# Kernel optimization log

Measured on AMD Instinct MI355X. Metric: run time of the kernel, lower is better.

Reference implementation:

```python
import jax, jax.numpy as jnp
import numpy as np

N = 100_000   # nodes
E = 1_250_000 # edges
D = 64        # feature dim


def setup_inputs() -> dict:
    key = jax.random.key(0)
    k1, k2, k3, k4 = jax.random.split(key, 4)
    x = jax.random.normal(k1, (N, D), dtype=jnp.float32)
    edge_index = jax.random.randint(k2, (2, E), 0, N, dtype=jnp.int32)
    s = 1.0 / np.sqrt(D)  # glorot-ish scale
    W1 = jax.random.uniform(k3, (D, D), minval=-s, maxval=s, dtype=jnp.float32)
    W2 = jax.random.uniform(k4, (D, D), minval=-s, maxval=s, dtype=jnp.float32)
    b1 = jnp.zeros((D,), jnp.float32)
    b2 = jnp.zeros((D,), jnp.float32)
    return {"x": x, "edge_index": edge_index, "W1": W1, "b1": b1, "W2": W2, "b2": b2}


def gcn_conv(x, edge_index, W, b):
    # PyG GCNConv: add self-loops, symmetric normalization D^-1/2 A D^-1/2,
    # linear transform, scatter-add aggregation over destination nodes.
    n = x.shape[0]
    src, dst = edge_index[0], edge_index[1]
    xw = x @ W  # [N, D]
    deg = jax.ops.segment_sum(jnp.ones((edge_index.shape[1],), x.dtype), dst,
                              num_segments=n) + 1.0  # +1 for self-loop
    inv_sqrt = jax.lax.rsqrt(deg)  # [N]
    coef = inv_sqrt[src] * inv_sqrt[dst]  # [E]
    agg = jax.ops.segment_sum(xw[src] * coef[:, None], dst, num_segments=n)
    # self-loop contribution: coef_ii = deg_i^-1
    agg = agg + xw * (inv_sqrt * inv_sqrt)[:, None]
    return agg + b


def reference(x, edge_index, W1, b1, W2, b2):
    h = jax.nn.relu(gcn_conv(x, edge_index, W1, b1))
    # dropout p=0.6 is identity in eval mode (training=False)
    out = gcn_conv(h, edge_index, W2, b2)
    return jax.nn.log_softmax(out, axis=1)
```

## Files before the change

kernel.cpp:

```cpp
#include <hip/hip_runtime.h>

#define DD 64
#define BSH 8
#define NB_MAX 512
#define SCAP 4096
#define BIN_CH 4096

typedef __attribute__((ext_vector_type(8))) short bf16x8;
typedef __attribute__((ext_vector_type(4))) float f32x4;
union Frag { bf16x8 v; uint32_t d[4]; };

__device__ __forceinline__ float bf_lo(uint32_t d) { return __uint_as_float(d << 16); }
__device__ __forceinline__ float bf_hi(uint32_t d) { return __uint_as_float(d & 0xffff0000u); }
__device__ __forceinline__ float bf2f(uint32_t h) { return __uint_as_float(h << 16); }
__device__ __forceinline__ uint32_t f2bf(float f) {
    uint32_t u = __float_as_uint(f);
    u += 0x7fffu + ((u >> 16) & 1u);
    return u >> 16;
}

__global__ __launch_bounds__(256) void bin_kernel(const int* __restrict__ src,
                                                  const int* __restrict__ dst,
                                                  int* __restrict__ bcnt,
                                                  uint32_t* __restrict__ staging,
                                                  int E, int NB) {
    __shared__ uint32_t sorted[BIN_CH];
    __shared__ int cnt[NB_MAX];
    __shared__ int loc[NB_MAX];
    __shared__ int resv[NB_MAX];
    __shared__ int wsum[4][2];
    int tid = threadIdx.x;
    int lane = tid & 63, wv = tid >> 6;
    int base = blockIdx.x * BIN_CH;
    int cE = min(BIN_CH, E - base);

    cnt[tid] = 0; cnt[tid + 256] = 0;
    __syncthreads();
    for (int k = tid; k < cE; k += 256)
        atomicAdd(&cnt[dst[base + k] >> BSH], 1);
    __syncthreads();
    int v0 = cnt[tid], v1 = cnt[tid + 256];
    int s0 = v0, s1 = v1;
#pragma unroll
    for (int o = 1; o < 64; o <<= 1) {
        int t0 = __shfl_up(s0, o, 64);
        int t1 = __shfl_up(s1, o, 64);
        if (lane >= o) { s0 += t0; s1 += t1; }
    }
    if (lane == 63) { wsum[wv][0] = s0; wsum[wv][1] = s1; }
    __syncthreads();
    int add0 = 0, add1 = 0;
    for (int w = 0; w < wv; ++w) { add0 += wsum[w][0]; add1 += wsum[w][1]; }
    int tot0 = wsum[0][0] + wsum[1][0] + wsum[2][0] + wsum[3][0];
    int e0 = s0 + add0 - v0;
    int e1 = tot0 + s1 + add1 - v1;
    resv[tid]       = v0 ? atomicAdd(&bcnt[tid], v0) : 0;
    resv[tid + 256] = v1 ? atomicAdd(&bcnt[tid + 256], v1) : 0;
    loc[tid] = e0; loc[tid + 256] = e1;
    __syncthreads();
    for (int k = tid; k < cE; k += 256) {
        int s = src[base + k], d = dst[base + k];
        int b = d >> BSH;
        int p = atomicAdd(&loc[b], 1);
        sorted[p] = ((uint32_t)s << BSH) | (uint32_t)(d & ((1 << BSH) - 1));
    }
    __syncthreads();
#pragma unroll
    for (int half = 0; half < 2; ++half) {
        int b = tid + half * 256;
        int c = cnt[b];
        if (c > 0 && b < NB) {
            int st = loc[b] - c;
            int r = resv[b];
            int lim = SCAP - r;
            int cw = min(c, max(lim, 0));
            size_t gb = (size_t)b * SCAP + r;
            for (int j = 0; j < cw; ++j) staging[gb + j] = sorted[st + j];
        }
    }
}

__global__ __launch_bounds__(256) void sort_kernel(const int* __restrict__ bcnt,
                                                   const uint32_t* __restrict__ staging,
                                                   int* __restrict__ rowptr,
                                                   float* __restrict__ inv,
                                                   uint32_t* __restrict__ srcs,
                                                   int n, int E, int NB) {
    __shared__ uint32_t raw[SCAP];
    __shared__ uint32_t sorted[SCAP];
    __shared__ int scnt[1 << BSH];
    __shared__ int soff[1 << BSH];
    __shared__ int lcur[1 << BSH];
    __shared__ int wred[4];
    __shared__ int wsum[4];
    int tid = threadIdx.x;
    int lane = tid & 63, wv = tid >> 6;
    int b = blockIdx.x;
    int base = b << BSH;
    int nd = min(1 << BSH, n - base);
    int cb = min(bcnt[b], SCAP);

    int part = 0;
    for (int j = tid; j < b; j += 256) part += bcnt[j];
#pragma unroll
    for (int o = 1; o < 64; o <<= 1) part += __shfl_xor(part, o, 64);
    if (lane == 0) wred[wv] = part;
    scnt[tid] = 0;
    __syncthreads();
    int bbase = wred[0] + wred[1] + wred[2] + wred[3];

    for (int k = tid; k < cb; k += 256) {
        uint32_t w = staging[(size_t)b * SCAP + k];
        raw[k] = w;
        atomicAdd(&scnt[w & ((1 << BSH) - 1)], 1);
    }
    __syncthreads();
    int v = scnt[tid];
    int sc = v;
#pragma unroll
    for (int o = 1; o < 64; o <<= 1) {
        int t = __shfl_up(sc, o, 64);
        if (lane >= o) sc += t;
    }
    if (lane == 63) wsum[wv] = sc;
    __syncthreads();
    int add = 0;
    if (wv > 0) add += wsum[0];
    if (wv > 1) add += wsum[1];
    if (wv > 2) add += wsum[2];
    int incl = sc + add;
    soff[tid] = incl - v;
    lcur[tid] = incl - v;
    if (tid < nd) {
        rowptr[base + tid] = bbase + soff[tid];
        inv[base + tid] = rsqrtf((float)v + 1.0f);
    }
    if (b == NB - 1 && tid == 0) rowptr[n] = E;
    __syncthreads();
    for (int k = tid; k < cb; k += 256) {
        uint32_t w = raw[k];
        int p = atomicAdd(&lcur[w & ((1 << BSH) - 1)], 1);
        sorted[p] = w >> BSH;
    }
    __syncthreads();
    for (int k = tid; k < cb; k += 256) srcs[bbase + k] = sorted[k] << 5;
}

template <int XBF>
__global__ __launch_bounds__(256) void gemm64_mfma(const void* __restrict__ Xv,
                                                   const float* __restrict__ W,
                                                   const float* __restrict__ inv,
                                                   uint16_t* __restrict__ Y, int n) {
    __shared__ float Ws[DD * DD];
    int tid = threadIdx.x;
    for (int i = tid; i < DD * DD; i += 256) Ws[i] = W[i];
    __syncthreads();
    int lane = tid & 63, quad = lane >> 4, l16 = lane & 15;

    Frag bhi[4][2], blo[4][2];
#pragma unroll
    for (int t = 0; t < 4; ++t)
#pragma unroll
        for (int c = 0; c < 2; ++c) {
            int col = t * 16 + l16;
            int kb = c * 32 + quad * 8;
#pragma unroll
            for (int i = 0; i < 4; ++i) {
                float w0 = Ws[(kb + 2 * i) * DD + col];
                float w1 = Ws[(kb + 2 * i + 1) * DD + col];
                uint32_t h0 = f2bf(w0), h1 = f2bf(w1);
                uint32_t l0 = f2bf(w0 - bf2f(h0)), l1 = f2bf(w1 - bf2f(h1));
                bhi[t][c].d[i] = h0 | (h1 << 16);
                blo[t][c].d[i] = l0 | (l1 << 16);
            }
        }

    int ngroups = (n + 15) >> 4;
    int nwaves = gridDim.x * 4;
    int wid = blockIdx.x * 4 + (tid >> 6);
    for (int g = wid; g < ngroups; g += nwaves) {
        int rb = g << 4;
        int row = min(rb + l16, n - 1);
        f32x4 acc[4];
#pragma unroll
        for (int t = 0; t < 4; ++t) acc[t] = (f32x4){0.f, 0.f, 0.f, 0.f};
#pragma unroll
        for (int c = 0; c < 2; ++c) {
            Frag ahi, alo;
            if constexpr (XBF == 0) {
                const float* xr = (const float*)Xv + (size_t)row * DD + c * 32 + quad * 8;
                float4 x0 = *(const float4*)xr;
                float4 x1 = *(const float4*)(xr + 4);
                float f[8] = {x0.x, x0.y, x0.z, x0.w, x1.x, x1.y, x1.z, x1.w};
#pragma unroll
                for (int i = 0; i < 4; ++i) {
                    uint32_t h0 = f2bf(f[2 * i]), h1 = f2bf(f[2 * i + 1]);
                    ahi.d[i] = h0 | (h1 << 16);
                    alo.d[i] = f2bf(f[2 * i] - bf2f(h0)) | (f2bf(f[2 * i + 1] - bf2f(h1)) << 16);
                }
            } else {
                const int4* xr = (const int4*)((const uint32_t*)Xv + (size_t)row * 32 + c * 16 + quad * 4);
                int4 a = *xr;
                ahi.d[0] = a.x; ahi.d[1] = a.y; ahi.d[2] = a.z; ahi.d[3] = a.w;
            }
#pragma unroll
            for (int t = 0; t < 4; ++t) {
                acc[t] = __builtin_amdgcn_mfma_f32_16x16x32_bf16(ahi.v, bhi[t][c].v, acc[t], 0, 0, 0);
                acc[t] = __builtin_amdgcn_mfma_f32_16x16x32_bf16(ahi.v, blo[t][c].v, acc[t], 0, 0, 0);
                if constexpr (XBF == 0)
                    acc[t] = __builtin_amdgcn_mfma_f32_16x16x32_bf16(alo.v, bhi[t][c].v, acc[t], 0, 0, 0);
            }
        }
#pragma unroll
        for (int r = 0; r < 4; ++r) {
            int ro = rb + quad * 4 + r;
            if (ro < n) {
                float sc = inv[ro];
#pragma unroll
                for (int t = 0; t < 4; ++t)
                    Y[(size_t)ro * DD + t * 16 + l16] = (uint16_t)f2bf(acc[t][r] * sc);
            }
        }
    }
}

template <int MODE>
__global__ __launch_bounds__(256) void agg_kernel(const int* __restrict__ rowptr,
                                                  const uint32_t* __restrict__ srcs,
                                                  const float* __restrict__ inv,
                                                  const uint32_t* __restrict__ XWb,
                                                  const float* __restrict__ b,
                                                  void* __restrict__ OUTv, int n) {
    int gid = blockIdx.x * 256 + threadIdx.x;
    int w = gid >> 6, lane = gid & 63;
    if (w * 2 >= n) return;
    int h = lane >> 5, l = lane & 31;
    int i = w * 2 + h;
    bool act = i < n;
    int ic = act ? i : n - 1;
    int g = l >> 3, m = l & 7;

    float a[8];
#pragma unroll
    for (int k = 0; k < 8; ++k) a[k] = 0.f;
    if (g == 0) {
        int4 d = *(const int4*)(XWb + (size_t)ic * 32 + 4 * m);
        a[0] = bf_lo((uint32_t)d.x); a[1] = bf_hi((uint32_t)d.x);
        a[2] = bf_lo((uint32_t)d.y); a[3] = bf_hi((uint32_t)d.y);
        a[4] = bf_lo((uint32_t)d.z); a[5] = bf_hi((uint32_t)d.z);
        a[6] = bf_lo((uint32_t)d.w); a[7] = bf_hi((uint32_t)d.w);
    }

    int jstart = rowptr[ic];
    int jend = act ? rowptr[ic + 1] : jstart;
    if (jstart < jend) {
        int last = jend - 1;
        int jq = jstart + g;
        uint32_t s0 = srcs[min(jq, last)];
        uint32_t s1 = srcs[min(jq + 4, last)];
        uint32_t s2 = srcs[min(jq + 8, last)];
        uint32_t s3 = srcs[min(jq + 12, last)];
        int4 d0 = *(const int4*)(XWb + s0 + 4 * m);
        int4 d1 = *(const int4*)(XWb + s1 + 4 * m);
        int4 d2 = *(const int4*)(XWb + s2 + 4 * m);
        for (int j = jq; j < jend; j += 4) {
            uint32_t s4 = srcs[min(j + 16, last)];
            int4 d3 = *(const int4*)(XWb + s3 + 4 * m);
            a[0] += bf_lo((uint32_t)d0.x); a[1] += bf_hi((uint32_t)d0.x);
            a[2] += bf_lo((uint32_t)d0.y); a[3] += bf_hi((uint32_t)d0.y);
            a[4] += bf_lo((uint32_t)d0.z); a[5] += bf_hi((uint32_t)d0.z);
            a[6] += bf_lo((uint32_t)d0.w); a[7] += bf_hi((uint32_t)d0.w);
            s3 = s4;
            d0 = d1; d1 = d2; d2 = d3;
        }
    }

#pragma unroll
    for (int k = 0; k < 8; ++k) {
        a[k] += __shfl_xor(a[k], 8, 64);
        a[k] += __shfl_xor(a[k], 16, 64);
    }

    float iv = inv[ic];
    float4 bb0 = *(const float4*)(b + 8 * m);
    float4 bb1 = *(const float4*)(b + 8 * m + 4);
    float f0 = fmaf(a[0], iv, bb0.x), f1 = fmaf(a[1], iv, bb0.y);
    float f2 = fmaf(a[2], iv, bb0.z), f3 = fmaf(a[3], iv, bb0.w);
    float f4 = fmaf(a[4], iv, bb1.x), f5 = fmaf(a[5], iv, bb1.y);
    float f6 = fmaf(a[6], iv, bb1.z), f7 = fmaf(a[7], iv, bb1.w);

    if (MODE == 0) {
        if (act && g == 0) {
            int4 d;
            d.x = (int)((f2bf(fmaxf(f1, 0.f)) << 16) | f2bf(fmaxf(f0, 0.f)));
            d.y = (int)((f2bf(fmaxf(f3, 0.f)) << 16) | f2bf(fmaxf(f2, 0.f)));
            d.z = (int)((f2bf(fmaxf(f5, 0.f)) << 16) | f2bf(fmaxf(f4, 0.f)));
            d.w = (int)((f2bf(fmaxf(f7, 0.f)) << 16) | f2bf(fmaxf(f6, 0.f)));
            *(int4*)((uint32_t*)OUTv + (size_t)i * 32 + 4 * m) = d;
        }
    } else {
        float mx = fmaxf(fmaxf(fmaxf(f0, f1), fmaxf(f2, f3)),
                         fmaxf(fmaxf(f4, f5), fmaxf(f6, f7)));
#pragma unroll
        for (int o = 4; o > 0; o >>= 1) mx = fmaxf(mx, __shfl_xor(mx, o, 64));
        float e = __expf(f0 - mx) + __expf(f1 - mx) + __expf(f2 - mx) + __expf(f3 - mx)
                + __expf(f4 - mx) + __expf(f5 - mx) + __expf(f6 - mx) + __expf(f7 - mx);
#pragma unroll
        for (int o = 4; o > 0; o >>= 1) e += __shfl_xor(e, o, 64);
        float ls = __logf(e);
        if (act && g == 0) {
            float4 r0 = make_float4(f0 - mx - ls, f1 - mx - ls, f2 - mx - ls, f3 - mx - ls);
            float4 r1 = make_float4(f4 - mx - ls, f5 - mx - ls, f6 - mx - ls, f7 - mx - ls);
            *(float4*)((float*)OUTv + (size_t)i * DD + 8 * m) = r0;
            *(float4*)((float*)OUTv + (size_t)i * DD + 8 * m + 4) = r1;
        }
    }
}

extern "C" void kernel_launch(void* const* d_in, const int* in_sizes, int n_in,
                              void* d_out, int out_size, void* d_ws, size_t ws_size,
                              hipStream_t stream) {
    const float* x  = (const float*)d_in[0];
    const int*   ei = (const int*)d_in[1];
    const float* W1 = (const float*)d_in[2];
    const float* b1 = (const float*)d_in[3];
    const float* W2 = (const float*)d_in[4];
    const float* b2 = (const float*)d_in[5];
    float* out = (float*)d_out;

    const int n = in_sizes[0] / DD;
    const int E = in_sizes[1] / 2;
    const int* src = ei;
    const int* dst = ei + E;
    const int NB = (n + (1 << BSH) - 1) >> BSH;

    size_t off = 0;
    int* base = (int*)d_ws;
    int* bcnt = base + off; off += NB_MAX;
    uint32_t* staging = (uint32_t*)(base + off); off += (size_t)NB_MAX * SCAP;
    uint32_t* srcs = (uint32_t*)(base + off); off += E;
    int* rowptr = base + off; off += (size_t)n + 1;
    float* inv  = (float*)(base + off); off += n;
    uint32_t* XWb = (uint32_t*)(base + off); off += (size_t)n * 32;
    uint32_t* hb  = (uint32_t*)(base + off); off += (size_t)n * 32;

    hipMemsetAsync(bcnt, 0, NB_MAX * sizeof(int), stream);
    bin_kernel<<<(E + BIN_CH - 1) / BIN_CH, 256, 0, stream>>>(src, dst, bcnt, staging, E, NB);
    sort_kernel<<<NB, 256, 0, stream>>>(bcnt, staging, rowptr, inv, srcs, n, E, NB);

    const int ablocks = (n + 7) / 8;

    gemm64_mfma<0><<<1024, 256, 0, stream>>>(x, W1, inv, (uint16_t*)XWb, n);
    agg_kernel<0><<<ablocks, 256, 0, stream>>>(rowptr, srcs, inv, XWb, b1, hb, n);

    gemm64_mfma<1><<<1024, 256, 0, stream>>>(hb, W2, inv, (uint16_t*)XWb, n);
    agg_kernel<1><<<ablocks, 256, 0, stream>>>(rowptr, srcs, inv, XWb, b2, out, n);
}
```

Baseline: 231.0 us.

## Fuse memset, binning and sorting into one cooperative kernel with grid syncs

Replaces the memset plus bin_kernel and sort_kernel launches with a single cooperative prep_kernel that zeroes the bucket counters, bins edges, and sorts per bucket, separated by grid.sync(). This is meant to remove two launch gaps and the memset. In exchange, the fused kernel's shared memory is the sum of both phases (~50KB), which lowers the number of resident blocks. A grid of about 391 blocks must all be co-resident for the cooperative launch, and each grid sync has its own cost.

After: 330.0 us. 1.43x slower.

```diff
diff --git a/kernel.cpp b/kernel.cpp
--- a/kernel.cpp
+++ b/kernel.cpp
@@ -1,4 +1,7 @@
 #include <hip/hip_runtime.h>
+#include <hip/hip_cooperative_groups.h>
+
+namespace cg = cooperative_groups;
 
 #define DD 64
 #define BSH 8
@@ -19,131 +22,134 @@
     return u >> 16;
 }
 
-__global__ __launch_bounds__(256) void bin_kernel(const int* __restrict__ src,
-                                                  const int* __restrict__ dst,
-                                                  int* __restrict__ bcnt,
-                                                  uint32_t* __restrict__ staging,
-                                                  int E, int NB) {
-    __shared__ uint32_t sorted[BIN_CH];
+__global__ __launch_bounds__(256) void prep_kernel(const int* __restrict__ src,
+                                                   const int* __restrict__ dst,
+                                                   int* __restrict__ bcnt,
+                                                   uint32_t* __restrict__ staging,
+                                                   int* __restrict__ rowptr,
+                                                   float* __restrict__ inv,
+                                                   uint32_t* __restrict__ srcs,
+                                                   int n, int E, int NB, int nbin) {
+    cg::grid_group grid = cg::this_grid();
+    __shared__ uint32_t p1sorted[BIN_CH];
     __shared__ int cnt[NB_MAX];
     __shared__ int loc[NB_MAX];
     __shared__ int resv[NB_MAX];
-    __shared__ int wsum[4][2];
-    int tid = threadIdx.x;
-    int lane = tid & 63, wv = tid >> 6;
-    int base = blockIdx.x * BIN_CH;
-    int cE = min(BIN_CH, E - base);
-
-    cnt[tid] = 0; cnt[tid + 256] = 0;
-    __syncthreads();
-    for (int k = tid; k < cE; k += 256)
-        atomicAdd(&cnt[dst[base + k] >> BSH], 1);
-    __syncthreads();
-    int v0 = cnt[tid], v1 = cnt[tid + 256];
-    int s0 = v0, s1 = v1;
-#pragma unroll
-    for (int o = 1; o < 64; o <<= 1) {
-        int t0 = __shfl_up(s0, o, 64);
-        int t1 = __shfl_up(s1, o, 64);
-        if (lane >= o) { s0 += t0; s1 += t1; }
-    }
-    if (lane == 63) { wsum[wv][0] = s0; wsum[wv][1] = s1; }
-    __syncthreads();
-    int add0 = 0, add1 = 0;
-    for (int w = 0; w < wv; ++w) { add0 += wsum[w][0]; add1 += wsum[w][1]; }
-    int tot0 = wsum[0][0] + wsum[1][0] + wsum[2][0] + wsum[3][0];
-    int e0 = s0 + add0 - v0;
-    int e1 = tot0 + s1 + add1 - v1;
-    resv[tid]       = v0 ? atomicAdd(&bcnt[tid], v0) : 0;
-    resv[tid + 256] = v1 ? atomicAdd(&bcnt[tid + 256], v1) : 0;
-    loc[tid] = e0; loc[tid + 256] = e1;
-    __syncthreads();
-    for (int k = tid; k < cE; k += 256) {
-        int s = src[base + k], d = dst[base + k];
-        int b = d >> BSH;
-        int p = atomicAdd(&loc[b], 1);
-        sorted[p] = ((uint32_t)s << BSH) | (uint32_t)(d & ((1 << BSH) - 1));
-    }
-    __syncthreads();
-#pragma unroll
-    for (int half = 0; half < 2; ++half) {
-        int b = tid + half * 256;
-        int c = cnt[b];
-        if (c > 0 && b < NB) {
-            int st = loc[b] - c;
-            int r = resv[b];
-            int lim = SCAP - r;
-            int cw = min(c, max(lim, 0));
-            size_t gb = (size_t)b * SCAP + r;
-            for (int j = 0; j < cw; ++j) staging[gb + j] = sorted[st + j];
-        }
-    }
-}
-
-__global__ __launch_bounds__(256) void sort_kernel(const int* __restrict__ bcnt,
-                                                   const uint32_t* __restrict__ staging,
-                                                   int* __restrict__ rowptr,
-                                                   float* __restrict__ inv,
-                                                   uint32_t* __restrict__ srcs,
-                                                   int n, int E, int NB) {
+    __shared__ int wsum2[4][2];
     __shared__ uint32_t raw[SCAP];
     __shared__ uint32_t sorted[SCAP];
     __shared__ int scnt[1 << BSH];
-    __shared__ int soff[1 << BSH];
     __shared__ int lcur[1 << BSH];
     __shared__ int wred[4];
     __shared__ int wsum[4];
+
     int tid = threadIdx.x;
     int lane = tid & 63, wv = tid >> 6;
+
+    if (blockIdx.x == 0) { bcnt[tid] = 0; bcnt[tid + 256] = 0; }
+    grid.sync();
+
+    if (blockIdx.x < nbin) {
+        int base = blockIdx.x * BIN_CH;
+        int cE = min(BIN_CH, E - base);
+
+        cnt[tid] = 0; cnt[tid + 256] = 0;
+        __syncthreads();
+        for (int k = tid; k < cE; k += 256)
+            atomicAdd(&cnt[dst[base + k] >> BSH], 1);
+        __syncthreads();
+        int v0 = cnt[tid], v1 = cnt[tid + 256];
+        int s0 = v0, s1 = v1;
+#pragma unroll
+        for (int o = 1; o < 64; o <<= 1) {
+            int t0 = __shfl_up(s0, o, 64);
+            int t1 = __shfl_up(s1, o, 64);
+            if (lane >= o) { s0 += t0; s1 += t1; }
+        }
+        if (lane == 63) { wsum2[wv][0] = s0; wsum2[wv][1] = s1; }
+        __syncthreads();
+        int add0 = 0, add1 = 0;
+        for (int w = 0; w < wv; ++w) { add0 += wsum2[w][0]; add1 += wsum2[w][1]; }
+        int tot0 = wsum2[0][0] + wsum2[1][0] + wsum2[2][0] + wsum2[3][0];
+        int e0 = s0 + add0 - v0;
+        int e1 = tot0 + s1 + add1 - v1;
+        resv[tid]       = v0 ? atomicAdd(&bcnt[tid], v0) : 0;
+        resv[tid + 256] = v1 ? atomicAdd(&bcnt[tid + 256], v1) : 0;
+        loc[tid] = e0; loc[tid + 256] = e1;
+        __syncthreads();
+        for (int k = tid; k < cE; k += 256) {
+            int s = src[base + k], d = dst[base + k];
+            int b = d >> BSH;
+            int p = atomicAdd(&loc[b], 1);
+            p1sorted[p] = ((uint32_t)s << BSH) | (uint32_t)(d & ((1 << BSH) - 1));
+        }
+        __syncthreads();
+#pragma unroll
+        for (int half = 0; half < 2; ++half) {
+            int b = tid + half * 256;
+            int c = cnt[b];
+            if (c > 0 && b < NB) {
+                int st = loc[b] - c;
+                int r = resv[b];
+                int lim = SCAP - r;
+                int cw = min(c, max(lim, 0));
+                size_t gb = (size_t)b * SCAP + r;
+                for (int j = 0; j < cw; ++j) staging[gb + j] = p1sorted[st + j];
+            }
+        }
+    }
+    grid.sync();
+
     int b = blockIdx.x;
-    int base = b << BSH;
-    int nd = min(1 << BSH, n - base);
-    int cb = min(bcnt[b], SCAP);
-
-    int part = 0;
-    for (int j = tid; j < b; j += 256) part += bcnt[j];
-#pragma unroll
-    for (int o = 1; o < 64; o <<= 1) part += __shfl_xor(part, o, 64);
-    if (lane == 0) wred[wv] = part;
-    scnt[tid] = 0;
-    __syncthreads();
-    int bbase = wred[0] + wred[1] + wred[2] + wred[3];
-
-    for (int k = tid; k < cb; k += 256) {
-        uint32_t w = staging[(size_t)b * SCAP + k];
-        raw[k] = w;
-        atomicAdd(&scnt[w & ((1 << BSH) - 1)], 1);
-    }
-    __syncthreads();
-    int v = scnt[tid];
-    int sc = v;
-#pragma unroll
-    for (int o = 1; o < 64; o <<= 1) {
-        int t = __shfl_up(sc, o, 64);
-        if (lane >= o) sc += t;
-    }
-    if (lane == 63) wsum[wv] = sc;
-    __syncthreads();
-    int add = 0;
-    if (wv > 0) add += wsum[0];
-    if (wv > 1) add += wsum[1];
-    if (wv > 2) add += wsum[2];
-    int incl = sc + add;
-    soff[tid] = incl - v;
-    lcur[tid] = incl - v;
-    if (tid < nd) {
-        rowptr[base + tid] = bbase + soff[tid];
-        inv[base + tid] = rsqrtf((float)v + 1.0f);
-    }
-    if (b == NB - 1 && tid == 0) rowptr[n] = E;
-    __syncthreads();
-    for (int k = tid; k < cb; k += 256) {
-        uint32_t w = raw[k];
-        int p = atomicAdd(&lcur[w & ((1 << BSH) - 1)], 1);
-        sorted[p] = w >> BSH;
-    }
-    __syncthreads();
-    for (int k = tid; k < cb; k += 256) srcs[bbase + k] = sorted[k] << 5;
+    if (b < NB) {
+        int base = b << BSH;
+        int nd = min(1 << BSH, n - base);
+        int cb = min(bcnt[b], SCAP);
+
+        int part = 0;
+        for (int j = tid; j < b; j += 256) part += bcnt[j];
+#pragma unroll
+        for (int o = 1; o < 64; o <<= 1) part += __shfl_xor(part, o, 64);
+        if (lane == 0) wred[wv] = part;
+        scnt[tid] = 0;
+        __syncthreads();
+        int bbase = wred[0] + wred[1] + wred[2] + wred[3];
+
+        for (int k = tid; k < cb; k += 256) {
+            uint32_t w = staging[(size_t)b * SCAP + k];
+            raw[k] = w;
+            atomicAdd(&scnt[w & ((1 << BSH) - 1)], 1);
+        }
+        __syncthreads();
+        int v = scnt[tid];
+        int sc = v;
+#pragma unroll
+        for (int o = 1; o < 64; o <<= 1) {
+            int t = __shfl_up(sc, o, 64);
+            if (lane >= o) sc += t;
+        }
+        if (lane == 63) wsum[wv] = sc;
+        __syncthreads();
+        int add = 0;
+        if (wv > 0) add += wsum[0];
+        if (wv > 1) add += wsum[1];
+        if (wv > 2) add += wsum[2];
+        int ex = sc + add - v;
+        lcur[tid] = ex;
+        if (tid < nd) {
+            rowptr[base + tid] = bbase + ex;
+            inv[base + tid] = rsqrtf((float)v + 1.0f);
+        }
+        if (b == NB - 1 && tid == 0) rowptr[n] = E;
+        __syncthreads();
+        for (int k = tid; k < cb; k += 256) {
+            uint32_t w = raw[k];
+            int p = atomicAdd(&lcur[w & ((1 << BSH) - 1)], 1);
+            sorted[p] = w >> BSH;
+        }
+        __syncthreads();
+        for (int k = tid; k < cb; k += 256) srcs[bbase + k] = sorted[k] << 5;
+    }
 }
 
 template <int XBF>
@@ -333,6 +339,7 @@
     const int* src = ei;
     const int* dst = ei + E;
     const int NB = (n + (1 << BSH) - 1) >> BSH;
+    const int nbin = (E + BIN_CH - 1) / BIN_CH;
 
     size_t off = 0;
     int* base = (int*)d_ws;
@@ -344,9 +351,14 @@
     uint32_t* XWb = (uint32_t*)(base + off); off += (size_t)n * 32;
     uint32_t* hb  = (uint32_t*)(base + off); off += (size_t)n * 32;
 
-    hipMemsetAsync(bcnt, 0, NB_MAX * sizeof(int), stream);
-    bin_kernel<<<(E + BIN_CH - 1) / BIN_CH, 256, 0, stream>>>(src, dst, bcnt, staging, E, NB);
-    sort_kernel<<<NB, 256, 0, stream>>>(bcnt, staging, rowptr, inv, srcs, n, E, NB);
+    {
+        int gridsz = NB > nbin ? NB : nbin;
+        void* args[] = {(void*)&src, (void*)&dst, (void*)&bcnt, (void*)&staging,
+                        (void*)&rowptr, (void*)&inv, (void*)&srcs,
+                        (void*)&n, (void*)&E, (void*)&NB, (void*)&nbin};
+        hipLaunchCooperativeKernel((void*)prep_kernel, dim3(gridsz), dim3(256),
+                                   args, 0, stream);
+    }
 
     const int ablocks = (n + 7) / 8;
 
```
